# Optimization experiments

Hardware: AMD Instinct MI355X
Metric: run time of the kernel (lower is better)

The kernel has to match this reference:

```python
import jax, jax.numpy as jnp
import numpy as np

VOCAB = 9
D = 128      # EMBED_DIM
S = 64       # SEQ_LEN / context_length
B = 512      # batch
NH = 4       # num_heads
DH = D // NH # head dim = 32
NB = 2       # num_blocks
EPS = 1e-5


def setup_inputs() -> dict:
    key = jax.random.key(0)
    ks = jax.random.split(key, 10)
    rn = lambda k, shape: jax.random.normal(k, shape, jnp.float32) * 0.02
    return {
        "x": jax.random.randint(ks[0], (B, S), 0, VOCAB),
        "emb": rn(ks[1], (VOCAB, D)),
        "ln1_w": jnp.ones((NB, D), jnp.float32),          # pre-sLSTM LayerNorm weight
        "Wg": rn(ks[2], (NB, 4, NH, DH, DH)),             # headwise gate projections (i,f,z,o)
        "R": rn(ks[3], (NB, NH, DH, 4 * DH)),             # recurrent kernels per head
        "bias": rn(ks[4], (NB, NH, 4, DH)),               # cell bias per head/gate
        "gn_w": jnp.ones((NB, D), jnp.float32),           # multi-head (group) norm weight
        "ln2_w": jnp.ones((NB, D), jnp.float32),          # pre-FF LayerNorm weight
        "ff_up_w": rn(ks[5], (NB, 2 * D, D)),             # gated FF up projection
        "ff_down_w": rn(ks[6], (NB, D, D)),               # FF down projection
        "post_w": jnp.ones((D,), jnp.float32),            # post-blocks LayerNorm weight
        "proj_w": rn(ks[7], (VOCAB, D)),
        "proj_b": jnp.zeros((VOCAB,), jnp.float32),
    }


def _layernorm(x, w):
    mu = x.mean(-1, keepdims=True)
    var = x.var(-1, keepdims=True)
    return (x - mu) * jax.lax.rsqrt(var + EPS) * w


def _mh_groupnorm(h, w):
    # h: [B,S,NH,DH] -> normalize over DH per head, scale by per-channel w [D]
    mu = h.mean(-1, keepdims=True)
    var = h.var(-1, keepdims=True)
    hn = (h - mu) * jax.lax.rsqrt(var + EPS)
    return hn.reshape(h.shape[0], h.shape[1], D) * w


def _slstm_layer(xh, Wg, R, b):
    # xh: [B,S,NH,DH]; Wg: [4,NH,DH,DH]; R: [NH,DH,4*DH]; b: [NH,4,DH]
    gx = jnp.einsum('bsnh,gnkh->sbngk', xh, Wg)  # [S,B,NH,4,DH] gate preacts (i,f,z,o)

    def step(carry, g):
        h, c, n, m = carry  # each [B,NH,DH]
        ry = jnp.einsum('bnh,nhk->bnk', h, R).reshape(h.shape[0], NH, 4, DH)
        raw = g + ry + b
        i_r, f_r, z_r, o_r = raw[:, :, 0], raw[:, :, 1], raw[:, :, 2], raw[:, :, 3]
        logfplusm = m + jax.nn.log_sigmoid(f_r)
        mnew = jnp.maximum(i_r, logfplusm)            # stabilizer
        ig = jnp.exp(i_r - mnew)
        fg = jnp.exp(logfplusm - mnew)
        cnew = fg * c + ig * jnp.tanh(z_r)
        nnew = fg * n + ig
        hnew = jax.nn.sigmoid(o_r) * cnew / nnew
        return (hnew, cnew, nnew, mnew), hnew

    z0 = jnp.zeros((xh.shape[0], NH, DH), xh.dtype)
    _, hs = jax.lax.scan(step, (z0, z0, z0, z0), gx)
    return hs.transpose(1, 0, 2, 3)  # [B,S,NH,DH]


def reference(x, emb, ln1_w, Wg, R, bias, gn_w, ln2_w, ff_up_w, ff_down_w, post_w, proj_w, proj_b):
    h = emb[x]  # [B,S,D]
    for bi in range(NB):
        xn = _layernorm(h, ln1_w[bi])
        y = _slstm_layer(xn.reshape(h.shape[0], S, NH, DH), Wg[bi], R[bi], bias[bi])
        h = h + _mh_groupnorm(y, gn_w[bi])
        xn = _layernorm(h, ln2_w[bi])
        up = xn @ ff_up_w[bi].T                       # [B,S,2D]
        gate, upv = up[..., :D], up[..., D:]
        h = h + (jax.nn.gelu(gate, approximate=False) * upv) @ ff_down_w[bi].T
    h = _layernorm(h, post_w)
    return h @ proj_w.T + proj_b  # [B,S,VOCAB]
```

## Files before the change

kernel.cpp:

```cpp
#include <hip/hip_runtime.h>
#include <math.h>

#define D      128
#define S_LEN  64
#define B_SZ   512
#define NH     4
#define DH     32
#define NB     2
#define VOCAB  9
#define EPS    1e-5f
#define NTOK   (B_SZ * S_LEN)

template <int CTRL>
__device__ __forceinline__ float dppf(float x) {
    return __int_as_float(__builtin_amdgcn_update_dpp(
        0, __float_as_int(x), CTRL, 0xF, 0xF, true));
}
__device__ __forceinline__ float wsum64(float x) {
    x += dppf<0x111>(x);
    x += dppf<0x112>(x);
    x += dppf<0x114>(x);
    x += dppf<0x118>(x);
    x += dppf<0x142>(x);
    x += dppf<0x143>(x);
    return __int_as_float(__builtin_amdgcn_readlane(__float_as_int(x), 63));
}

__device__ __forceinline__ int xc3(int t, int c) { return c ^ (((t >> 1) & 7) << 2); }
__device__ __forceinline__ int xa (int t, int c) { return c ^ ((t & 7) << 2); }
__device__ __forceinline__ int xg (int c)        { return c ^ ((c >> 5) << 3); }

__global__ __launch_bounds__(256) void k_embed(const int* __restrict__ x,
                                               const float* __restrict__ emb,
                                               float* __restrict__ h,
                                               float* __restrict__ stats)
{
    int lane = threadIdx.x & 63;
    int wv   = threadIdx.x >> 6;
    int tok  = blockIdx.x * 4 + wv;
    int xi   = x[tok];
    float2 v = ((const float2*)(emb + xi * D))[lane];
    ((float2*)(h + (size_t)tok * D))[lane] = v;
    float s1 = wsum64(v.x + v.y);
    float s2 = wsum64(v.x * v.x + v.y * v.y);
    float mu  = s1 * (1.0f / D);
    float var = s2 * (1.0f / D) - mu * mu;
    if (lane == 0) {
        stats[tok * 2]     = mu;
        stats[tok * 2 + 1] = rsqrtf(var + EPS);
    }
}

__global__ __launch_bounds__(256, 2) void k_gx(const float* __restrict__ Wg,
                                               const float* __restrict__ bias,
                                               const float* __restrict__ lnw,
                                               const float* __restrict__ h,
                                               const float* __restrict__ stats,
                                               float* __restrict__ gx)
{
    __shared__ float xs[32 * 128];
    __shared__ float wl[4 * 32 * 128];

    int tid  = threadIdx.x;
    int lane = tid & 63;
    int wv   = tid >> 6;
    size_t tok0 = (size_t)blockIdx.x * 32;

    {
        int q = tid & 7;
        #pragma unroll
        for (int it = 0; it < 16; ++it) {
            int row = it * 32 + (tid >> 3);
            int g  = row >> 7;
            int n  = (row >> 5) & 3;
            int hh = row & 31;
            float4 v = *(const float4*)(Wg + row * 32 + q * 4);
            int col = g * 32 + hh;
            int sw  = q << 2;
            float* dst = wl + n * 4096;
            dst[(q * 4 + 0) * 128 + (col ^ sw)] = v.x;
            dst[(q * 4 + 1) * 128 + (col ^ sw)] = v.y;
            dst[(q * 4 + 2) * 128 + (col ^ sw)] = v.z;
            dst[(q * 4 + 3) * 128 + (col ^ sw)] = v.w;
        }
    }
    for (int i = 0; i < 8; ++i) {
        int t = wv * 8 + i;
        const float* hp = h + (tok0 + t) * D;
        float mu = stats[(tok0 + t) * 2];
        float rs = stats[(tok0 + t) * 2 + 1];
        float v1 = (hp[lane]      - mu) * rs * lnw[lane];
        float v2 = (hp[64 + lane] - mu) * rs * lnw[64 + lane];
        xs[t * 128 + xg(lane)]      = v1;
        xs[t * 128 + xg(lane + 64)] = v2;
    }
    __syncthreads();

    int nh   = lane >> 4;
    int col0 = (lane & 15) * 8;
    int t0   = wv * 8;

    float acc[8][8];
    #pragma unroll
    for (int j = 0; j < 8; ++j)
        #pragma unroll
        for (int cc = 0; cc < 8; ++cc) acc[j][cc] = 0.f;

    const float* wbase = wl + nh * 4096;
    #pragma unroll
    for (int k4 = 0; k4 < 8; ++k4) {
        int sw  = k4 << 2;
        int ac4 = (nh * 32 + k4 * 4) ^ (nh << 3);
        float4 w0[4], w1[4];
        #pragma unroll
        for (int i = 0; i < 4; ++i) {
            int k = k4 * 4 + i;
            w0[i] = *(const float4*)&wbase[k * 128 + (col0 ^ sw)];
            w1[i] = *(const float4*)&wbase[k * 128 + ((col0 + 4) ^ sw)];
        }
        #pragma unroll
        for (int j = 0; j < 8; ++j) {
            float4 a4 = *(const float4*)&xs[(t0 + j) * 128 + ac4];
            #pragma unroll
            for (int i = 0; i < 4; ++i) {
                float a = ((const float*)&a4)[i];
                acc[j][0] = fmaf(a, w0[i].x, acc[j][0]);
                acc[j][1] = fmaf(a, w0[i].y, acc[j][1]);
                acc[j][2] = fmaf(a, w0[i].z, acc[j][2]);
                acc[j][3] = fmaf(a, w0[i].w, acc[j][3]);
                acc[j][4] = fmaf(a, w1[i].x, acc[j][4]);
                acc[j][5] = fmaf(a, w1[i].y, acc[j][5]);
                acc[j][6] = fmaf(a, w1[i].z, acc[j][6]);
                acc[j][7] = fmaf(a, w1[i].w, acc[j][7]);
            }
        }
    }

    float4 bb0 = *(const float4*)(bias + nh * 128 + col0);
    float4 bb1 = *(const float4*)(bias + nh * 128 + col0 + 4);
    #pragma unroll
    for (int j = 0; j < 8; ++j) {
        int gt = (int)tok0 + t0 + j;
        int bb = gt >> 6;
        int ss = gt & 63;
        float* op = gx + ((size_t)(bb * NH + nh) * S_LEN + ss) * 128 + col0;
        float4 o0v, o1v;
        o0v.x = acc[j][0] + bb0.x; o0v.y = acc[j][1] + bb0.y;
        o0v.z = acc[j][2] + bb0.z; o0v.w = acc[j][3] + bb0.w;
        o1v.x = acc[j][4] + bb1.x; o1v.y = acc[j][5] + bb1.y;
        o1v.z = acc[j][6] + bb1.z; o1v.w = acc[j][7] + bb1.w;
        *(float4*)op       = o0v;
        *(float4*)(op + 4) = o1v;
    }
}

__global__ __launch_bounds__(64, 2) void k_scan(const float* __restrict__ Rm,
                                                const float* __restrict__ gnw,
                                                const float* __restrict__ gx,
                                                float* __restrict__ h)
{
    __shared__ float WA[8][64][4];
    __shared__ float WB[8][64][4];

    int b    = blockIdx.x >> 2;
    int n    = blockIdx.x & 3;
    int lane = threadIdx.x;
    int e    = lane >> 1;
    int sub  = lane & 1;
    int colA = sub * DH + e;

    #pragma unroll
    for (int cc = 0; cc < 8; ++cc) {
        float4 a, bv;
        #pragma unroll
        for (int j = 0; j < 4; ++j) {
            ((float*)&a)[j]  = Rm[(n * DH + cc * 4 + j) * 128 + colA];
            ((float*)&bv)[j] = Rm[(n * DH + cc * 4 + j) * 128 + 64 + colA];
        }
        *(float4*)WA[cc][lane] = a;
        *(float4*)WB[cc][lane] = bv;
    }
    float gw = gnw[n * DH + e];
    __syncthreads();

    float c = 0.f, nacc = 0.f, m = 0.f;
    float hu[DH];
    #pragma unroll
    for (int i = 0; i < DH; ++i) hu[i] = 0.f;

    float* hb = h + ((size_t)b * S_LEN) * D + n * DH;
    const float* gxp = gx + ((size_t)(b * NH + n) * S_LEN) * 128;

    float pGA[4], pGB[4], pHR[4];
    #pragma unroll
    for (int k = 0; k < 4; ++k) {
        pGA[k] = gxp[k * 128 + colA];
        pGB[k] = gxp[k * 128 + 64 + colA];
        pHR[k] = hb[k * D + e];
    }

    #pragma unroll 4
    for (int s = 0; s < S_LEN; ++s) {
        int sp = (s + 4 < S_LEN) ? s + 4 : S_LEN - 1;
        float nGA = gxp[sp * 128 + colA];
        float nGB = gxp[sp * 128 + 64 + colA];
        float nHR = hb[sp * D + e];

        float r0=0,r1=0,r2=0,r3=0,q0=0,q1=0,q2=0,q3=0;
        #pragma unroll
        for (int cc = 0; cc < 8; ++cc) {
            float4 wa = *(const float4*)WA[cc][lane];
            float4 wb = *(const float4*)WB[cc][lane];
            r0 = fmaf(hu[cc*4+0], wa.x, r0);
            r1 = fmaf(hu[cc*4+1], wa.y, r1);
            r2 = fmaf(hu[cc*4+2], wa.z, r2);
            r3 = fmaf(hu[cc*4+3], wa.w, r3);
            q0 = fmaf(hu[cc*4+0], wb.x, q0);
            q1 = fmaf(hu[cc*4+1], wb.y, q1);
            q2 = fmaf(hu[cc*4+2], wb.z, q2);
            q3 = fmaf(hu[cc*4+3], wb.w, q3);
        }
        float rawA = pGA[0] + ((r0 + r1) + (r2 + r3));
        float rawB = pGB[0] + ((q0 + q1) + (q2 + q3));

        float xA = dppf<0xB1>(rawA);
        float xB = dppf<0xB1>(rawB);
        float i_r = sub ? xA   : rawA;
        float f_r = sub ? rawA : xA;
        float z_r = sub ? xB   : rawB;
        float o_r = sub ? rawB : xB;

        float lsf  = fminf(f_r, 0.f)
                   - 0.69314718055994531f * __log2f(1.0f + __expf(-fabsf(f_r)));
        float lfm  = m + lsf;
        float mnew = fmaxf(i_r, lfm);
        float ig   = __expf(i_r - mnew);
        float fg   = __expf(lfm - mnew);
        float t    = __expf(2.f * z_r);
        float tz   = 1.f - 2.f / (t + 1.f);
        c    = fg * c + ig * tz;
        nacc = fg * nacc + ig;
        m    = mnew;
        float hv = c / (nacc * (1.f + __expf(-o_r)));

        float s1 = wsum64(hv);
        float s2 = wsum64(hv * hv);
        float mu  = s1 * (1.f / 64.f);
        float var = s2 * (1.f / 64.f) - mu * mu;
        float hn  = (hv - mu) * rsqrtf(var + EPS) * gw;

        if (!sub) hb[s * D + e] = pHR[0] + hn;

        #pragma unroll
        for (int i = 0; i < DH; ++i)
            hu[i] = __int_as_float(
                __builtin_amdgcn_readlane(__float_as_int(hv), 2 * i));

        pGA[0]=pGA[1]; pGA[1]=pGA[2]; pGA[2]=pGA[3]; pGA[3]=nGA;
        pGB[0]=pGB[1]; pGB[1]=pGB[2]; pGB[2]=pGB[3]; pGB[3]=nGB;
        pHR[0]=pHR[1]; pHR[1]=pHR[2]; pHR[2]=pHR[3]; pHR[3]=nHR;
    }
}

template <int LAST>
__global__ __launch_bounds__(256, 3) void k_ff(float* __restrict__ h,
                                               const float* __restrict__ ln2w,
                                               const float* __restrict__ wup,
                                               const float* __restrict__ wdn,
                                               float* __restrict__ stats_out,
                                               const float* __restrict__ lastw,
                                               const float* __restrict__ projw,
                                               const float* __restrict__ projb,
                                               float* __restrict__ out)
{
    __shared__ float xs[32 * 128];
    __shared__ float as_[32 * 64];
    __shared__ float wt[2 * 32 * 64];

    int tid  = threadIdx.x;
    int lane = tid & 63;
    int wv   = tid >> 6;
    size_t tok0 = (size_t)blockIdx.x * 32;

    for (int i = 0; i < 8; ++i) {
        int t = wv * 8 + i;
        const float* hp = h + (tok0 + t) * D;
        float v1 = hp[lane], v2 = hp[64 + lane];
        float s1 = wsum64(v1 + v2);
        float s2 = wsum64(v1 * v1 + v2 * v2);
        float mu = s1 * (1.0f / D);
        float rs = rsqrtf(s2 * (1.0f / D) - mu * mu + EPS);
        xs[t * D + xc3(t, lane)]      = (v1 - mu) * rs * ln2w[lane];
        xs[t * D + xc3(t, lane + 64)] = (v2 - mu) * rs * ln2w[64 + lane];
    }

    int q     = tid & 7;
    int r0    = tid >> 3;
    int goff0 = r0 * D + q * 4;
    int goff1 = (r0 + 32) * D + q * 4;
    int s0    = r0 ^ (q << 2);
    int kb    = q * 4;

    auto ffld = [&](int id, float4* pre) {
        int p = (id >= 6) ? 1 : 0;
        int j = id - p * 6;
        const float* b0;
        const float* b1;
        if (j < 4) { b0 = wup + (p * 64) * D + j * 32;
                     b1 = wup + (128 + p * 64) * D + j * 32; }
        else       { int jj = j - 4;
                     b0 = wdn + p * 64 + jj * 32;
                     b1 = wdn + 64 * D + p * 64 + jj * 32; }
        pre[0] = *(const float4*)(b0 + goff0);
        pre[1] = *(const float4*)(b0 + goff1);
        pre[2] = *(const float4*)(b1 + goff0);
        pre[3] = *(const float4*)(b1 + goff1);
    };
    auto fst = [&](const float4* pre) {
        #pragma unroll
        for (int cc = 0; cc < 4; ++cc) {
            const float* p0 = (const float*)&pre[0];
            const float* p1 = (const float*)&pre[1];
            const float* p2 = (const float*)&pre[2];
            const float* p3 = (const float*)&pre[3];
            wt[(kb + cc) * 64 + s0]           = p0[cc];
            wt[(kb + cc) * 64 + s0 + 32]      = p1[cc];
            wt[2048 + (kb + cc) * 64 + s0]      = p2[cc];
            wt[2048 + (kb + cc) * 64 + s0 + 32] = p3[cc];
        }
    };

    int ti = tid >> 4;
    int oi = tid & 15;
    int t0 = ti * 2;
    int o0 = oi * 4;

    float accd[2][2][4];
    #pragma unroll
    for (int a1 = 0; a1 < 2; ++a1)
        #pragma unroll
        for (int j = 0; j < 2; ++j)
            #pragma unroll
            for (int cc = 0; cc < 4; ++cc) accd[a1][j][cc] = 0.f;

    float4 pre[4];
    ffld(0, pre);
    int id = 1;

    #pragma unroll
    for (int p = 0; p < 2; ++p) {
        float accg[2][4], accv[2][4];
        #pragma unroll
        for (int j = 0; j < 2; ++j)
            #pragma unroll
            for (int cc = 0; cc < 4; ++cc) { accg[j][cc] = 0.f; accv[j][cc] = 0.f; }

        for (int c4 = 0; c4 < 4; ++c4) {
            __syncthreads();
            fst(pre);
            if (id < 12) ffld(id, pre);
            ++id;
            __syncthreads();
            int kc = c4 * 32;
            #pragma unroll
            for (int k4 = 0; k4 < 8; ++k4) {
                float4 a0 = *(const float4*)&xs[t0 * D + xc3(t0, kc + k4 * 4)];
                float4 a1v = *(const float4*)&xs[(t0 + 1) * D + xc3(t0 + 1, kc + k4 * 4)];
                int ws = k4 << 2;
                #pragma unroll
                for (int i = 0; i < 4; ++i) {
                    int k = k4 * 4 + i;
                    float4 bg = *(const float4*)&wt[k * 64 + (o0 ^ ws)];
                    float4 bv = *(const float4*)&wt[2048 + k * 64 + (o0 ^ ws)];
                    float ax0 = ((const float*)&a0)[i];
                    float ax1 = ((const float*)&a1v)[i];
                    accg[0][0] = fmaf(ax0, bg.x, accg[0][0]);
                    accg[0][1] = fmaf(ax0, bg.y, accg[0][1]);
                    accg[0][2] = fmaf(ax0, bg.z, accg[0][2]);
                    accg[0][3] = fmaf(ax0, bg.w, accg[0][3]);
                    accg[1][0] = fmaf(ax1, bg.x, accg[1][0]);
                    accg[1][1] = fmaf(ax1, bg.y, accg[1][1]);
                    accg[1][2] = fmaf(ax1, bg.z, accg[1][2]);
                    accg[1][3] = fmaf(ax1, bg.w, accg[1][3]);
                    accv[0][0] = fmaf(ax0, bv.x, accv[0][0]);
                    accv[0][1] = fmaf(ax0, bv.y, accv[0][1]);
                    accv[0][2] = fmaf(ax0, bv.z, accv[0][2]);
                    accv[0][3] = fmaf(ax0, bv.w, accv[0][3]);
                    accv[1][0] = fmaf(ax1, bv.x, accv[1][0]);
                    accv[1][1] = fmaf(ax1, bv.y, accv[1][1]);
                    accv[1][2] = fmaf(ax1, bv.z, accv[1][2]);
                    accv[1][3] = fmaf(ax1, bv.w, accv[1][3]);
                }
            }
        }
        #pragma unroll
        for (int j = 0; j < 2; ++j) {
            int t = t0 + j;
            float4 av;
            float* ap = (float*)&av;
            #pragma unroll
            for (int cc = 0; cc < 4; ++cc) {
                float g = accg[j][cc];
                float u = accv[j][cc];
                ap[cc] = 0.5f * g * (1.0f + erff(g * 0.70710678118654752f)) * u;
            }
            *(float4*)&as_[t * 64 + xa(t, o0)] = av;
        }
        for (int c2 = 0; c2 < 2; ++c2) {
            __syncthreads();
            fst(pre);
            if (id < 12) ffld(id, pre);
            ++id;
            __syncthreads();
            int kc = c2 * 32;
            #pragma unroll
            for (int k4 = 0; k4 < 8; ++k4) {
                float4 a0 = *(const float4*)&as_[t0 * 64 + xa(t0, kc + k4 * 4)];
                float4 a1v = *(const float4*)&as_[(t0 + 1) * 64 + xa(t0 + 1, kc + k4 * 4)];
                int ws = k4 << 2;
                #pragma unroll
                for (int i = 0; i < 4; ++i) {
                    int k = k4 * 4 + i;
                    float4 b0v = *(const float4*)&wt[k * 64 + (o0 ^ ws)];
                    float4 b1v = *(const float4*)&wt[2048 + k * 64 + (o0 ^ ws)];
                    float ax0 = ((const float*)&a0)[i];
                    float ax1 = ((const float*)&a1v)[i];
                    accd[0][0][0] = fmaf(ax0, b0v.x, accd[0][0][0]);
                    accd[0][0][1] = fmaf(ax0, b0v.y, accd[0][0][1]);
                    accd[0][0][2] = fmaf(ax0, b0v.z, accd[0][0][2]);
                    accd[0][0][3] = fmaf(ax0, b0v.w, accd[0][0][3]);
                    accd[0][1][0] = fmaf(ax1, b0v.x, accd[0][1][0]);
                    accd[0][1][1] = fmaf(ax1, b0v.y, accd[0][1][1]);
                    accd[0][1][2] = fmaf(ax1, b0v.z, accd[0][1][2]);
                    accd[0][1][3] = fmaf(ax1, b0v.w, accd[0][1][3]);
                    accd[1][0][0] = fmaf(ax0, b1v.x, accd[1][0][0]);
                    accd[1][0][1] = fmaf(ax0, b1v.y, accd[1][0][1]);
                    accd[1][0][2] = fmaf(ax0, b1v.z, accd[1][0][2]);
                    accd[1][0][3] = fmaf(ax0, b1v.w, accd[1][0][3]);
                    accd[1][1][0] = fmaf(ax1, b1v.x, accd[1][1][0]);
                    accd[1][1][1] = fmaf(ax1, b1v.y, accd[1][1][1]);
                    accd[1][1][2] = fmaf(ax1, b1v.z, accd[1][1][2]);
                    accd[1][1][3] = fmaf(ax1, b1v.w, accd[1][1][3]);
                }
            }
        }
    }

    #pragma unroll
    for (int j = 0; j < 2; ++j) {
        int t = t0 + j;
        size_t tok = tok0 + t;
        #pragma unroll
        for (int a1 = 0; a1 < 2; ++a1) {
            int cb = a1 * 64 + o0;
            float4 hres = *(const float4*)(h + tok * D + cb);
            float4 hn;
            hn.x = hres.x + accd[a1][j][0];
            hn.y = hres.y + accd[a1][j][1];
            hn.z = hres.z + accd[a1][j][2];
            hn.w = hres.w + accd[a1][j][3];
            if (!LAST) *(float4*)(h + tok * D + cb) = hn;
            *(float4*)&xs[t * D + xc3(t, cb)] = hn;
        }
    }
    __syncthreads();

    if (!LAST) {
        for (int i = 0; i < 8; ++i) {
            int t = wv * 8 + i;
            float v1 = xs[t * D + xc3(t, lane)];
            float v2 = xs[t * D + xc3(t, lane + 64)];
            float s1 = wsum64(v1 + v2);
            float s2 = wsum64(v1 * v1 + v2 * v2);
            float mu = s1 * (1.0f / D);
            float rs = rsqrtf(s2 * (1.0f / D) - mu * mu + EPS);
            if (lane == 0) {
                stats_out[(tok0 + t) * 2]     = mu;
                stats_out[(tok0 + t) * 2 + 1] = rs;
            }
        }
    } else {
        float pw1[VOCAB], pw2[VOCAB], pb[VOCAB];
        #pragma unroll
        for (int v = 0; v < VOCAB; ++v) {
            pw1[v] = projw[v * D + lane];
            pw2[v] = projw[v * D + 64 + lane];
            pb[v]  = projb[v];
        }
        for (int i = 0; i < 8; ++i) {
            int t = wv * 8 + i;
            float v1 = xs[t * D + xc3(t, lane)];
            float v2 = xs[t * D + xc3(t, lane + 64)];
            float s1 = wsum64(v1 + v2);
            float s2 = wsum64(v1 * v1 + v2 * v2);
            float mu = s1 * (1.0f / D);
            float rs = rsqrtf(s2 * (1.0f / D) - mu * mu + EPS);
            float x1 = (v1 - mu) * rs * lastw[lane];
            float x2 = (v2 - mu) * rs * lastw[64 + lane];
            #pragma unroll
            for (int v = 0; v < VOCAB; ++v) {
                float pp = wsum64(fmaf(x1, pw1[v], x2 * pw2[v]));
                if (lane == 0) out[(tok0 + t) * VOCAB + v] = pp + pb[v];
            }
        }
    }
}

extern "C" void kernel_launch(void* const* d_in, const int* in_sizes, int n_in,
                              void* d_out, int out_size, void* d_ws, size_t ws_size,
                              hipStream_t stream)
{
    const int*   x     = (const int*)  d_in[0];
    const float* emb   = (const float*)d_in[1];
    const float* ln1   = (const float*)d_in[2];
    const float* Wg    = (const float*)d_in[3];
    const float* Rm    = (const float*)d_in[4];
    const float* bias  = (const float*)d_in[5];
    const float* gnw   = (const float*)d_in[6];
    const float* ln2   = (const float*)d_in[7];
    const float* wup   = (const float*)d_in[8];
    const float* wdn   = (const float*)d_in[9];
    const float* postw = (const float*)d_in[10];
    const float* projw = (const float*)d_in[11];
    const float* projb = (const float*)d_in[12];
    float* out   = (float*)d_out;
    float* hbuf  = (float*)d_ws;
    float* stats = hbuf + (size_t)NTOK * D;
    float* gxbuf = stats + (size_t)NTOK * 2;

    k_embed<<<NTOK / 4, 256, 0, stream>>>(x, emb, hbuf, stats);

    for (int bi = 0; bi < NB; ++bi) {
        k_gx<<<NTOK / 32, 256, 0, stream>>>(Wg + bi * 4 * NH * DH * DH,
                                            bias + bi * NH * 4 * DH,
                                            ln1 + bi * D,
                                            hbuf, stats, gxbuf);
        k_scan<<<B_SZ * NH, 64, 0, stream>>>(Rm + bi * NH * DH * 4 * DH,
                                             gnw + bi * D,
                                             gxbuf, hbuf);
        if (bi == 0)
            k_ff<0><<<NTOK / 32, 256, 0, stream>>>(hbuf, ln2 + bi * D,
                                                   wup + bi * 2 * D * D,
                                                   wdn + bi * D * D,
                                                   stats, nullptr, nullptr,
                                                   nullptr, nullptr);
        else
            k_ff<1><<<NTOK / 32, 256, 0, stream>>>(hbuf, ln2 + bi * D,
                                                   wup + bi * 2 * D * D,
                                                   wdn + bi * D * D,
                                                   nullptr, postw, projw,
                                                   projb, out);
    }
}
```

Measured before the change: 390.3 us.

## Keep recurrent weights in registers and retile FF GEMM to 64-token blocks

```diff
diff --git a/kernel.cpp b/kernel.cpp
--- a/kernel.cpp
+++ b/kernel.cpp
@@ -11,6 +11,8 @@
 #define EPS    1e-5f
 #define NTOK   (B_SZ * S_LEN)
 
+#define XS_STRIDE 132
+
 template <int CTRL>
 __device__ __forceinline__ float dppf(float x) {
     return __int_as_float(__builtin_amdgcn_update_dpp(
@@ -25,10 +27,8 @@
     x += dppf<0x143>(x);
     return __int_as_float(__builtin_amdgcn_readlane(__float_as_int(x), 63));
 }
-
-__device__ __forceinline__ int xc3(int t, int c) { return c ^ (((t >> 1) & 7) << 2); }
-__device__ __forceinline__ int xa (int t, int c) { return c ^ ((t & 7) << 2); }
-__device__ __forceinline__ int xg (int c)        { return c ^ ((c >> 5) << 3); }
+__device__ __forceinline__ int swz(int o) { return o ^ (((o >> 5) & 3) << 2); }
+__device__ __forceinline__ int xg (int c) { return c ^ ((c >> 5) << 3); }
 
 __global__ __launch_bounds__(256) void k_embed(const int* __restrict__ x,
                                                const float* __restrict__ emb,
@@ -154,14 +154,11 @@
     }
 }
 
-__global__ __launch_bounds__(64, 2) void k_scan(const float* __restrict__ Rm,
+__global__ __launch_bounds__(64, 1) void k_scan(const float* __restrict__ Rm,
                                                 const float* __restrict__ gnw,
                                                 const float* __restrict__ gx,
                                                 float* __restrict__ h)
 {
-    __shared__ float WA[8][64][4];
-    __shared__ float WB[8][64][4];
-
     int b    = blockIdx.x >> 2;
     int n    = blockIdx.x & 3;
     int lane = threadIdx.x;
@@ -169,19 +166,18 @@
     int sub  = lane & 1;
     int colA = sub * DH + e;
 
-    #pragma unroll
-    for (int cc = 0; cc < 8; ++cc) {
-        float4 a, bv;
-        #pragma unroll
-        for (int j = 0; j < 4; ++j) {
-            ((float*)&a)[j]  = Rm[(n * DH + cc * 4 + j) * 128 + colA];
-            ((float*)&bv)[j] = Rm[(n * DH + cc * 4 + j) * 128 + 64 + colA];
-        }
-        *(float4*)WA[cc][lane] = a;
-        *(float4*)WB[cc][lane] = bv;
+    float RA[DH], RB[DH];
+    #pragma unroll
+    for (int i = 0; i < DH; ++i) {
+        RA[i] = Rm[(n * DH + i) * 128 + colA];
+        RB[i] = Rm[(n * DH + i) * 128 + 64 + colA];
+    }
+    #pragma unroll
+    for (int i = 0; i < DH; ++i) {
+        asm volatile("" : "+v"(RA[i]));
+        asm volatile("" : "+v"(RB[i]));
     }
     float gw = gnw[n * DH + e];
-    __syncthreads();
 
     float c = 0.f, nacc = 0.f, m = 0.f;
     float hu[DH];
@@ -199,7 +195,6 @@
         pHR[k] = hb[k * D + e];
     }
 
-    #pragma unroll 4
     for (int s = 0; s < S_LEN; ++s) {
         int sp = (s + 4 < S_LEN) ? s + 4 : S_LEN - 1;
         float nGA = gxp[sp * 128 + colA];
@@ -208,17 +203,15 @@
 
         float r0=0,r1=0,r2=0,r3=0,q0=0,q1=0,q2=0,q3=0;
         #pragma unroll
-        for (int cc = 0; cc < 8; ++cc) {
-            float4 wa = *(const float4*)WA[cc][lane];
-            float4 wb = *(const float4*)WB[cc][lane];
-            r0 = fmaf(hu[cc*4+0], wa.x, r0);
-            r1 = fmaf(hu[cc*4+1], wa.y, r1);
-            r2 = fmaf(hu[cc*4+2], wa.z, r2);
-            r3 = fmaf(hu[cc*4+3], wa.w, r3);
-            q0 = fmaf(hu[cc*4+0], wb.x, q0);
-            q1 = fmaf(hu[cc*4+1], wb.y, q1);
-            q2 = fmaf(hu[cc*4+2], wb.z, q2);
-            q3 = fmaf(hu[cc*4+3], wb.w, q3);
+        for (int i = 0; i < DH; i += 4) {
+            r0 = fmaf(hu[i],   RA[i],   r0);
+            r1 = fmaf(hu[i+1], RA[i+1], r1);
+            r2 = fmaf(hu[i+2], RA[i+2], r2);
+            r3 = fmaf(hu[i+3], RA[i+3], r3);
+            q0 = fmaf(hu[i],   RB[i],   q0);
+            q1 = fmaf(hu[i+1], RB[i+1], q1);
+            q2 = fmaf(hu[i+2], RB[i+2], q2);
+            q3 = fmaf(hu[i+3], RB[i+3], q3);
         }
         float rawA = pGA[0] + ((r0 + r1) + (r2 + r3));
         float rawB = pGB[0] + ((q0 + q1) + (q2 + q3));
@@ -263,7 +256,7 @@
 }
 
 template <int LAST>
-__global__ __launch_bounds__(256, 3) void k_ff(float* __restrict__ h,
+__global__ __launch_bounds__(256, 1) void k_ff(float* __restrict__ h,
                                                const float* __restrict__ ln2w,
                                                const float* __restrict__ wup,
                                                const float* __restrict__ wdn,
@@ -273,203 +266,191 @@
                                                const float* __restrict__ projb,
                                                float* __restrict__ out)
 {
-    __shared__ float xs[32 * 128];
-    __shared__ float as_[32 * 64];
-    __shared__ float wt[2 * 32 * 64];
+    __shared__ float xs[64 * XS_STRIDE];
+    __shared__ float wt[32 * 256];
 
     int tid  = threadIdx.x;
     int lane = tid & 63;
     int wv   = tid >> 6;
-    size_t tok0 = (size_t)blockIdx.x * 32;
-
-    for (int i = 0; i < 8; ++i) {
-        int t = wv * 8 + i;
+    size_t tok0 = (size_t)blockIdx.x * 64;
+
+    int ti = tid >> 4;
+    int oi = tid & 15;
+    int o0 = oi * 8;
+    int og = swz(o0);
+    int srow_u = swz(tid);
+    int srow_d = swz(tid >> 1);
+
+    float4 pre[8];
+    auto ffld_up = [&](int c) {
+        const float* p = wup + tid * 128 + c * 32;
+        #pragma unroll
+        for (int q = 0; q < 8; ++q) pre[q] = *(const float4*)(p + q * 4);
+    };
+    auto fst_up = [&]() {
+        #pragma unroll
+        for (int q = 0; q < 8; ++q)
+            #pragma unroll
+            for (int jj = 0; jj < 4; ++jj)
+                wt[(q * 4 + jj) * 256 + srow_u] = ((const float*)&pre[q])[jj];
+    };
+    auto ffld_dn = [&](int c) {
+        const float* p = wdn + (tid >> 1) * 128 + c * 32 + (tid & 1) * 16;
+        #pragma unroll
+        for (int q = 0; q < 4; ++q) pre[q] = *(const float4*)(p + q * 4);
+    };
+    auto fst_dn = [&]() {
+        int kb = (tid & 1) * 16;
+        #pragma unroll
+        for (int q = 0; q < 4; ++q)
+            #pragma unroll
+            for (int jj = 0; jj < 4; ++jj)
+                wt[(kb + q * 4 + jj) * 128 + srow_d] = ((const float*)&pre[q])[jj];
+    };
+
+    ffld_up(0);
+    for (int i = 0; i < 16; ++i) {
+        int t = wv * 16 + i;
         const float* hp = h + (tok0 + t) * D;
         float v1 = hp[lane], v2 = hp[64 + lane];
         float s1 = wsum64(v1 + v2);
         float s2 = wsum64(v1 * v1 + v2 * v2);
         float mu = s1 * (1.0f / D);
         float rs = rsqrtf(s2 * (1.0f / D) - mu * mu + EPS);
-        xs[t * D + xc3(t, lane)]      = (v1 - mu) * rs * ln2w[lane];
-        xs[t * D + xc3(t, lane + 64)] = (v2 - mu) * rs * ln2w[64 + lane];
-    }
-
-    int q     = tid & 7;
-    int r0    = tid >> 3;
-    int goff0 = r0 * D + q * 4;
-    int goff1 = (r0 + 32) * D + q * 4;
-    int s0    = r0 ^ (q << 2);
-    int kb    = q * 4;
-
-    auto ffld = [&](int id, float4* pre) {
-        int p = (id >= 6) ? 1 : 0;
-        int j = id - p * 6;
-        const float* b0;
-        const float* b1;
-        if (j < 4) { b0 = wup + (p * 64) * D + j * 32;
-                     b1 = wup + (128 + p * 64) * D + j * 32; }
-        else       { int jj = j - 4;
-                     b0 = wdn + p * 64 + jj * 32;
-                     b1 = wdn + 64 * D + p * 64 + jj * 32; }
-        pre[0] = *(const float4*)(b0 + goff0);
-        pre[1] = *(const float4*)(b0 + goff1);
-        pre[2] = *(const float4*)(b1 + goff0);
-        pre[3] = *(const float4*)(b1 + goff1);
-    };
-    auto fst = [&](const float4* pre) {
-        #pragma unroll
-        for (int cc = 0; cc < 4; ++cc) {
-            const float* p0 = (const float*)&pre[0];
-            const float* p1 = (const float*)&pre[1];
-            const float* p2 = (const float*)&pre[2];
-            const float* p3 = (const float*)&pre[3];
-            wt[(kb + cc) * 64 + s0]           = p0[cc];
-            wt[(kb + cc) * 64 + s0 + 32]      = p1[cc];
-            wt[2048 + (kb + cc) * 64 + s0]      = p2[cc];
-            wt[2048 + (kb + cc) * 64 + s0 + 32] = p3[cc];
-        }
-    };
-
-    int ti = tid >> 4;
-    int oi = tid & 15;
-    int t0 = ti * 2;
-    int o0 = oi * 4;
-
-    float accd[2][2][4];
-    #pragma unroll
-    for (int a1 = 0; a1 < 2; ++a1)
-        #pragma unroll
-        for (int j = 0; j < 2; ++j)
-            #pragma unroll
-            for (int cc = 0; cc < 4; ++cc) accd[a1][j][cc] = 0.f;
-
-    float4 pre[4];
-    ffld(0, pre);
-    int id = 1;
-
-    #pragma unroll
-    for (int p = 0; p < 2; ++p) {
-        float accg[2][4], accv[2][4];
-        #pragma unroll
-        for (int j = 0; j < 2; ++j)
-            #pragma unroll
-            for (int cc = 0; cc < 4; ++cc) { accg[j][cc] = 0.f; accv[j][cc] = 0.f; }
-
-        for (int c4 = 0; c4 < 4; ++c4) {
-            __syncthreads();
-            fst(pre);
-            if (id < 12) ffld(id, pre);
-            ++id;
-            __syncthreads();
-            int kc = c4 * 32;
-            #pragma unroll
-            for (int k4 = 0; k4 < 8; ++k4) {
-                float4 a0 = *(const float4*)&xs[t0 * D + xc3(t0, kc + k4 * 4)];
-                float4 a1v = *(const float4*)&xs[(t0 + 1) * D + xc3(t0 + 1, kc + k4 * 4)];
-                int ws = k4 << 2;
+        xs[t * XS_STRIDE + lane]      = (v1 - mu) * rs * ln2w[lane];
+        xs[t * XS_STRIDE + 64 + lane] = (v2 - mu) * rs * ln2w[64 + lane];
+    }
+    fst_up();
+    ffld_up(1);
+    __syncthreads();
+
+    float accg[4][8], accv[4][8];
+    #pragma unroll
+    for (int j = 0; j < 4; ++j)
+        #pragma unroll
+        for (int cc = 0; cc < 8; ++cc) { accg[j][cc] = 0.f; accv[j][cc] = 0.f; }
+
+    for (int c = 0; c < 4; ++c) {
+        const float* xsp = xs + (ti * 4) * XS_STRIDE + c * 32;
+        #pragma unroll
+        for (int k4 = 0; k4 < 8; ++k4) {
+            float4 a[4];
+            #pragma unroll
+            for (int j = 0; j < 4; ++j)
+                a[j] = *(const float4*)&xsp[j * XS_STRIDE + k4 * 4];
+            #pragma unroll
+            for (int i = 0; i < 4; ++i) {
+                const float* wr = wt + (k4 * 4 + i) * 256;
+                float4 g0 = *(const float4*)&wr[og];
+                float4 g1 = *(const float4*)&wr[og + 4];
+                float4 v0 = *(const float4*)&wr[128 + og];
+                float4 v1 = *(const float4*)&wr[128 + og + 4];
                 #pragma unroll
-                for (int i = 0; i < 4; ++i) {
-                    int k = k4 * 4 + i;
-                    float4 bg = *(const float4*)&wt[k * 64 + (o0 ^ ws)];
-                    float4 bv = *(const float4*)&wt[2048 + k * 64 + (o0 ^ ws)];
-                    float ax0 = ((const float*)&a0)[i];
-                    float ax1 = ((const float*)&a1v)[i];
-                    accg[0][0] = fmaf(ax0, bg.x, accg[0][0]);
-                    accg[0][1] = fmaf(ax0, bg.y, accg[0][1]);
-                    accg[0][2] = fmaf(ax0, bg.z, accg[0][2]);
-                    accg[0][3] = fmaf(ax0, bg.w, accg[0][3]);
-                    accg[1][0] = fmaf(ax1, bg.x, accg[1][0]);
-                    accg[1][1] = fmaf(ax1, bg.y, accg[1][1]);
-                    accg[1][2] = fmaf(ax1, bg.z, accg[1][2]);
-                    accg[1][3] = fmaf(ax1, bg.w, accg[1][3]);
-                    accv[0][0] = fmaf(ax0, bv.x, accv[0][0]);
-                    accv[0][1] = fmaf(ax0, bv.y, accv[0][1]);
-                    accv[0][2] = fmaf(ax0, bv.z, accv[0][2]);
-                    accv[0][3] = fmaf(ax0, bv.w, accv[0][3]);
-                    accv[1][0] = fmaf(ax1, bv.x, accv[1][0]);
-                    accv[1][1] = fmaf(ax1, bv.y, accv[1][1]);
-                    accv[1][2] = fmaf(ax1, bv.z, accv[1][2]);
-                    accv[1][3] = fmaf(ax1, bv.w, accv[1][3]);
+                for (int j = 0; j < 4; ++j) {
+                    float av = ((const float*)&a[j])[i];
+                    accg[j][0] = fmaf(av, g0.x, accg[j][0]);
+                    accg[j][1] = fmaf(av, g0.y, accg[j][1]);
+                    accg[j][2] = fmaf(av, g0.z, accg[j][2]);
+                    accg[j][3] = fmaf(av, g0.w, accg[j][3]);
+                    accg[j][4] = fmaf(av, g1.x, accg[j][4]);
+                    accg[j][5] = fmaf(av, g1.y, accg[j][5]);
+                    accg[j][6] = fmaf(av, g1.z, accg[j][6]);
+                    accg[j][7] = fmaf(av, g1.w, accg[j][7]);
+                    accv[j][0] = fmaf(av, v0.x, accv[j][0]);
+                    accv[j][1] = fmaf(av, v0.y, accv[j][1]);
+                    accv[j][2] = fmaf(av, v0.z, accv[j][2]);
+                    accv[j][3] = fmaf(av, v0.w, accv[j][3]);
+                    accv[j][4] = fmaf(av, v1.x, accv[j][4]);
+                    accv[j][5] = fmaf(av, v1.y, accv[j][5]);
+                    accv[j][6] = fmaf(av, v1.z, accv[j][6]);
+                    accv[j][7] = fmaf(av, v1.w, accv[j][7]);
                 }
             }
         }
-        #pragma unroll
-        for (int j = 0; j < 2; ++j) {
-            int t = t0 + j;
-            float4 av;
-            float* ap = (float*)&av;
-            #pragma unroll
-            for (int cc = 0; cc < 4; ++cc) {
-                float g = accg[j][cc];
-                float u = accv[j][cc];
-                ap[cc] = 0.5f * g * (1.0f + erff(g * 0.70710678118654752f)) * u;
-            }
-            *(float4*)&as_[t * 64 + xa(t, o0)] = av;
-        }
-        for (int c2 = 0; c2 < 2; ++c2) {
-            __syncthreads();
-            fst(pre);
-            if (id < 12) ffld(id, pre);
-            ++id;
-            __syncthreads();
-            int kc = c2 * 32;
-            #pragma unroll
-            for (int k4 = 0; k4 < 8; ++k4) {
-                float4 a0 = *(const float4*)&as_[t0 * 64 + xa(t0, kc + k4 * 4)];
-                float4 a1v = *(const float4*)&as_[(t0 + 1) * 64 + xa(t0 + 1, kc + k4 * 4)];
-                int ws = k4 << 2;
+        __syncthreads();
+        if (c < 3)      { fst_up(); ffld_up(c + 2 <= 3 ? c + 2 : 3); if (c == 2) ffld_dn(0); }
+        else            {  }
+        if (c < 3) __syncthreads();
+    }
+
+    #pragma unroll
+    for (int j = 0; j < 4; ++j) {
+        int t = ti * 4 + j;
+        float av[8];
+        #pragma unroll
+        for (int cc = 0; cc < 8; ++cc) {
+            float g = accg[j][cc];
+            av[cc] = 0.5f * g * (1.0f + erff(g * 0.70710678118654752f)) * accv[j][cc];
+        }
+        *(float4*)&xs[t * XS_STRIDE + o0]     = *(float4*)&av[0];
+        *(float4*)&xs[t * XS_STRIDE + o0 + 4] = *(float4*)&av[4];
+    }
+    fst_dn();
+    ffld_dn(1);
+    __syncthreads();
+
+    float accd[4][8];
+    #pragma unroll
+    for (int j = 0; j < 4; ++j)
+        #pragma unroll
+        for (int cc = 0; cc < 8; ++cc) accd[j][cc] = 0.f;
+
+    for (int c = 0; c < 4; ++c) {
+        const float* xsp = xs + (ti * 4) * XS_STRIDE + c * 32;
+        #pragma unroll
+        for (int k4 = 0; k4 < 8; ++k4) {
+            float4 a[4];
+            #pragma unroll
+            for (int j = 0; j < 4; ++j)
+                a[j] = *(const float4*)&xsp[j * XS_STRIDE + k4 * 4];
+            #pragma unroll
+            for (int i = 0; i < 4; ++i) {
+                const float* wr = wt + (k4 * 4 + i) * 128;
+                float4 b0 = *(const float4*)&wr[og];
+                float4 b1 = *(const float4*)&wr[og + 4];
                 #pragma unroll
-                for (int i = 0; i < 4; ++i) {
-                    int k = k4 * 4 + i;
-                    float4 b0v = *(const float4*)&wt[k * 64 + (o0 ^ ws)];
-                    float4 b1v = *(const float4*)&wt[2048 + k * 64 + (o0 ^ ws)];
-                    float ax0 = ((const float*)&a0)[i];
-                    float ax1 = ((const float*)&a1v)[i];
-                    accd[0][0][0] = fmaf(ax0, b0v.x, accd[0][0][0]);
-                    accd[0][0][1] = fmaf(ax0, b0v.y, accd[0][0][1]);
-                    accd[0][0][2] = fmaf(ax0, b0v.z, accd[0][0][2]);
-                    accd[0][0][3] = fmaf(ax0, b0v.w, accd[0][0][3]);
-                    accd[0][1][0] = fmaf(ax1, b0v.x, accd[0][1][0]);
-                    accd[0][1][1] = fmaf(ax1, b0v.y, accd[0][1][1]);
-                    accd[0][1][2] = fmaf(ax1, b0v.z, accd[0][1][2]);
-                    accd[0][1][3] = fmaf(ax1, b0v.w, accd[0][1][3]);
-                    accd[1][0][0] = fmaf(ax0, b1v.x, accd[1][0][0]);
-                    accd[1][0][1] = fmaf(ax0, b1v.y, accd[1][0][1]);
-                    accd[1][0][2] = fmaf(ax0, b1v.z, accd[1][0][2]);
-                    accd[1][0][3] = fmaf(ax0, b1v.w, accd[1][0][3]);
-                    accd[1][1][0] = fmaf(ax1, b1v.x, accd[1][1][0]);
-                    accd[1][1][1] = fmaf(ax1, b1v.y, accd[1][1][1]);
-                    accd[1][1][2] = fmaf(ax1, b1v.z, accd[1][1][2]);
-                    accd[1][1][3] = fmaf(ax1, b1v.w, accd[1][1][3]);
+                for (int j = 0; j < 4; ++j) {
+                    float av = ((const float*)&a[j])[i];
+                    accd[j][0] = fmaf(av, b0.x, accd[j][0]);
+                    accd[j][1] = fmaf(av, b0.y, accd[j][1]);
+                    accd[j][2] = fmaf(av, b0.z, accd[j][2]);
+                    accd[j][3] = fmaf(av, b0.w, accd[j][3]);
+                    accd[j][4] = fmaf(av, b1.x, accd[j][4]);
+                    accd[j][5] = fmaf(av, b1.y, accd[j][5]);
+                    accd[j][6] = fmaf(av, b1.z, accd[j][6]);
+                    accd[j][7] = fmaf(av, b1.w, accd[j][7]);
                 }
             }
         }
-    }
-
-    #pragma unroll
-    for (int j = 0; j < 2; ++j) {
-        int t = t0 + j;
+        __syncthreads();
+        if (c < 3) { fst_dn(); ffld_dn(c + 2 <= 3 ? c + 2 : 3); __syncthreads(); }
+    }
+
+    #pragma unroll
+    for (int j = 0; j < 4; ++j) {
+        int t = ti * 4 + j;
         size_t tok = tok0 + t;
-        #pragma unroll
-        for (int a1 = 0; a1 < 2; ++a1) {
-            int cb = a1 * 64 + o0;
-            float4 hres = *(const float4*)(h + tok * D + cb);
-            float4 hn;
-            hn.x = hres.x + accd[a1][j][0];
-            hn.y = hres.y + accd[a1][j][1];
-            hn.z = hres.z + accd[a1][j][2];
-            hn.w = hres.w + accd[a1][j][3];
-            if (!LAST) *(float4*)(h + tok * D + cb) = hn;
-            *(float4*)&xs[t * D + xc3(t, cb)] = hn;
-        }
+        float4 h0 = *(const float4*)(h + tok * D + o0);
+        float4 h1 = *(const float4*)(h + tok * D + o0 + 4);
+        float4 n0, n1;
+        n0.x = h0.x + accd[j][0]; n0.y = h0.y + accd[j][1];
+        n0.z = h0.z + accd[j][2]; n0.w = h0.w + accd[j][3];
+        n1.x = h1.x + accd[j][4]; n1.y = h1.y + accd[j][5];
+        n1.z = h1.z + accd[j][6]; n1.w = h1.w + accd[j][7];
+        if (!LAST) {
+            *(float4*)(h + tok * D + o0)     = n0;
+            *(float4*)(h + tok * D + o0 + 4) = n1;
+        }
+        *(float4*)&xs[t * XS_STRIDE + o0]     = n0;
+        *(float4*)&xs[t * XS_STRIDE + o0 + 4] = n1;
     }
     __syncthreads();
 
     if (!LAST) {
-        for (int i = 0; i < 8; ++i) {
-            int t = wv * 8 + i;
-            float v1 = xs[t * D + xc3(t, lane)];
-            float v2 = xs[t * D + xc3(t, lane + 64)];
+        for (int i = 0; i < 16; ++i) {
+            int t = wv * 16 + i;
+            float v1 = xs[t * XS_STRIDE + lane];
+            float v2 = xs[t * XS_STRIDE + 64 + lane];
             float s1 = wsum64(v1 + v2);
             float s2 = wsum64(v1 * v1 + v2 * v2);
             float mu = s1 * (1.0f / D);
@@ -487,10 +468,10 @@
             pw2[v] = projw[v * D + 64 + lane];
             pb[v]  = projb[v];
         }
-        for (int i = 0; i < 8; ++i) {
-            int t = wv * 8 + i;
-            float v1 = xs[t * D + xc3(t, lane)];
-            float v2 = xs[t * D + xc3(t, lane + 64)];
+        for (int i = 0; i < 16; ++i) {
+            int t = wv * 16 + i;
+            float v1 = xs[t * XS_STRIDE + lane];
+            float v2 = xs[t * XS_STRIDE + 64 + lane];
             float s1 = wsum64(v1 + v2);
             float s2 = wsum64(v1 * v1 + v2 * v2);
             float mu = s1 * (1.0f / D);
@@ -539,13 +520,13 @@
                                              gnw + bi * D,
                                              gxbuf, hbuf);
         if (bi == 0)
-            k_ff<0><<<NTOK / 32, 256, 0, stream>>>(hbuf, ln2 + bi * D,
+            k_ff<0><<<NTOK / 64, 256, 0, stream>>>(hbuf, ln2 + bi * D,
                                                    wup + bi * 2 * D * D,
                                                    wdn + bi * D * D,
                                                    stats, nullptr, nullptr,
                                                    nullptr, nullptr);
         else
-            k_ff<1><<<NTOK / 32, 256, 0, stream>>>(hbuf, ln2 + bi * D,
+            k_ff<1><<<NTOK / 64, 256, 0, stream>>>(hbuf, ln2 + bi * D,
                                                    wup + bi * 2 * D * D,
                                                    wdn + bi * D * D,
                                                    nullptr, postw, projw,
```

Measured after the change: 845.0 us. 2.17x slower.
